# Kernel optimization log

Hardware: AMD Instinct MI355X
Metric: run time of the kernel (lower is better)

The kernel has to match this reference:

```python
import jax, jax.numpy as jnp
import numpy as np

EPS = 1e-6
INF = jnp.float32(1e12)
LAM = 1.0    # self.lam in RHD
ALPHA = 0.5  # 'alpha' is undefined in the original buggy forward; standard RHD uses 0.5


def _edt_sq_last(f):
    # Exact 1D squared distance transform along the last axis via min-plus
    # with the parabola cost (i-j)^2. f: [..., n] -> [..., n].
    n = f.shape[-1]
    idx = jnp.arange(n, dtype=f.dtype)
    d2 = (idx[:, None] - idx[None, :]) ** 2  # [n, n]
    return jnp.min(f[..., None, :] + d2, axis=-1)


def edt_sq(mask):
    # Squared Euclidean distance to nearest False pixel (scipy distance_transform_edt**2).
    # mask: bool [B, H, W]. Batched via lax.map to bound the [H, W, W] intermediate.
    f = jnp.where(mask, INF, jnp.float32(0.0))

    def one(fb):  # fb: [H, W]
        g = _edt_sq_last(fb)                 # pass along W
        d2 = _edt_sq_last(g.T).T             # pass along H
        return jnp.minimum(d2, INF)

    d2 = jax.lax.map(one, f)
    # compute_dtm leaves the map at 0 when the foreground mask is empty
    any_fg = jnp.any(mask, axis=(1, 2))
    return jnp.where(any_fg[:, None, None], d2, jnp.float32(0.0))


def setup_inputs() -> dict:
    key = jax.random.key(0)
    k1, k2 = jax.random.split(key)
    B, C, H, W = 8, 2, 512, 512
    logits = jax.random.normal(k1, (B, C, H, W), dtype=jnp.float32)
    outputs = jax.nn.softmax(logits, axis=1)  # module expects softmax results
    lab = jax.random.randint(k2, (B, H, W), 0, 2, dtype=jnp.int32)
    label_batch = jnp.stack([1 - lab, lab], axis=1)  # (B, 2, H, W) one-hot
    return {"outputs": outputs, "label_batch": label_batch}


def reference(outputs, label_batch):
    lab1_i = label_batch[:, 1]                      # (B, H, W) int
    lab1 = lab1_i.astype(outputs.dtype)

    # ---- HD loss (distance maps are constants: computed under no_grad) ----
    gt_d2 = edt_sq(lab1_i > 0)                      # (B, H, W) squared DTM of GT
    seg_d2 = edt_sq(outputs[:, 1] > 0.5)            # squared DTM of thresholded seg
    delta_s = (outputs[:, 1] - lab1) ** 2
    hd_loss = jnp.mean(delta_s * (seg_d2 + gt_d2))

    # ---- Dice loss on foreground channel ----
    score = outputs[:, 1]
    intersect = jnp.sum(score * lab1)
    denom = jnp.sum(score * score) + jnp.sum(lab1 * lab1)
    dice_loss = 1.0 - (2.0 * intersect + EPS) / (denom + EPS)

    # ---- Cross entropy: F.cross_entropy(outputs, label_batch[:,1].long()) ----
    logp = jax.nn.log_softmax(outputs, axis=1)      # (B, 2, H, W)
    picked = jnp.take_along_axis(logp, lab1_i[:, None].astype(jnp.int32), axis=1)[:, 0]
    ce_loss = -jnp.mean(picked)

    return LAM * (ce_loss + dice_loss) + (1.0 - ALPHA) * hd_loss
```

## Files before the change

### kernel.cpp

```cpp
#include <hip/hip_runtime.h>
#include <math.h>
#include <stdint.h>

#define INF_F 1.0e12f
#define NB 8
#define HW 512
#define PLANE (HW*HW)
#define NPIX (NB*PLANE)

__device__ __attribute__((noinline)) int exactRecompute(
    const float* __restrict__ outputs, const int* __restrict__ labels,
    int b, int z, int y, int x)
{
  const int base = (b*2 + 1)*PLANE;
  int m = 0x7fffffff;
  for (int ady = 0; ady < HW; ++ady) {
    if (ady*ady >= m) break;
    for (int sgn = 0; sgn < 2; ++sgn) {
      if (sgn && ady == 0) break;
      const int yy = sgn ? (y - ady) : (y + ady);
      if (yy < 0 || yy >= HW) continue;
      const int rb = base + yy*HW;
      const int a2 = ady*ady;
      for (int t = 0; t < HW; ++t) {
        const int c2 = a2 + t*t;
        if (c2 >= m) break;
        bool hit = false;
        const int xl = x - t, xr = x + t;
        if (xl >= 0)
          hit = (z == 0) ? (labels[rb + xl] <= 0) : !(outputs[rb + xl] > 0.5f);
        if (!hit && xr < HW)
          hit = (z == 0) ? (labels[rb + xr] <= 0) : !(outputs[rb + xr] > 0.5f);
        if (hit) { m = c2; break; }
      }
    }
  }
  return m;
}

__device__ __forceinline__ void visitRow(uint64_t w, int px, int a2,
                                         int pL2, int pR2, int& m, int& U)
{
  const uint64_t below = w & (~0ULL >> (63 - px));
  const uint64_t above = w >> px;
  if (below) { const int dL = px - (63 - __builtin_clzll(below)); m = min(m, a2 + dL*dL); }
  else        U = min(U, a2 + pL2);
  if (above) { const int dR = __builtin_ctzll(above); m = min(m, a2 + dR*dR); }
  else        U = min(U, a2 + pR2);
}

__device__ __forceinline__ float scanPixel(const uint64_t* __restrict__ W,
    int ry, int px, const float* __restrict__ outputs, const int* __restrict__ labels,
    int b, int z, int y, int x)
{
  const int pL2 = (px + 1)*(px + 1);
  const int pR2 = (48 - px)*(48 - px);
  int m = 0x7fffffff, U = 0x7fffffff;
  visitRow(W[ry], px, 0, pL2, pR2, m, U);
  int ady = 1;
  for (; ady <= 8; ++ady) {
    const int a2 = ady*ady;
    if (a2 >= m) break;
    visitRow(W[ry - ady], px, a2, pL2, pR2, m, U);
    visitRow(W[ry + ady], px, a2, pL2, pR2, m, U);
  }
  if (ady == 9) U = min(U, 81);
  if (m > U) {
    m = exactRecompute(outputs, labels, b, z, y, x);
    if (m == 0x7fffffff) return INF_F;
  }
  return (float)m;
}

__global__ __launch_bounds__(256) void fused_loss(
    const float* __restrict__ outputs, const int* __restrict__ labels,
    double* __restrict__ accum)
{
  __shared__ unsigned short l16[2][48][4];
  __shared__ uint64_t W[2][48];
  __shared__ double wred[4][5];
  const int tid = threadIdx.x;
  const int x0 = blockIdx.x * 32, y0 = blockIdx.y * 32, b = blockIdx.z;
  const int base1 = (b*2 + 1)*PLANE;

  for (int idx = tid; idx < 288; idx += 256) {
    const int z = idx / 144, rem = idx % 144;
    const int row = rem / 3, ch = rem % 3;
    const int yy = y0 - 8 + row;
    const int xs = x0 - 8 + ch*16;
    uint32_t bits = 0;
    if (yy >= 0 && yy < HW) {
      const int rb = base1 + yy*HW;
      if (xs >= 0 && xs + 16 <= HW) {
        if (z == 0) {
          const int4* p = (const int4*)(labels + rb + xs);
          const int4 a = p[0], c = p[1], d = p[2], e = p[3];
          const int v[16] = {a.x,a.y,a.z,a.w, c.x,c.y,c.z,c.w,
                             d.x,d.y,d.z,d.w, e.x,e.y,e.z,e.w};
#pragma unroll
          for (int t = 0; t < 16; ++t) if (v[t] <= 0) bits |= (1u << t);
        } else {
          const float4* p = (const float4*)(outputs + rb + xs);
          const float4 a = p[0], c = p[1], d = p[2], e = p[3];
          const float v[16] = {a.x,a.y,a.z,a.w, c.x,c.y,c.z,c.w,
                               d.x,d.y,d.z,d.w, e.x,e.y,e.z,e.w};
#pragma unroll
          for (int t = 0; t < 16; ++t) if (!(v[t] > 0.5f)) bits |= (1u << t);
        }
      } else {
        for (int t = 0; t < 16; ++t) {
          const int xx = xs + t;
          if (xx < 0 || xx >= HW) continue;
          const bool bg = (z == 0) ? (labels[rb + xx] <= 0)
                                   : !(outputs[rb + xx] > 0.5f);
          if (bg) bits |= (1u << t);
        }
      }
    }
    l16[z][row][ch] = (unsigned short)bits;
  }
  __syncthreads();
  if (tid < 96) {
    const int z = tid / 48, row = tid % 48;
    W[z][row] = (uint64_t)l16[z][row][0]
              | ((uint64_t)l16[z][row][1] << 16)
              | ((uint64_t)l16[z][row][2] << 32);
  }
  __syncthreads();

  const int lx = tid & 31, lyb = tid >> 5;
  const int px = 8 + lx;
  const int x = x0 + lx;
  double part = 0, dI = 0, dP2 = 0, dLs = 0, dCE = 0;
#pragma unroll
  for (int k = 0; k < 4; ++k) {
    const int ly = lyb + 8*k;
    const int y = y0 + ly;
    const int ry = 8 + ly;
    const float d2g = scanPixel(W[0], ry, px, outputs, labels, b, 0, y, x);
    const float d2s = scanPixel(W[1], ry, px, outputs, labels, b, 1, y, x);
    const int off = base1 + y*HW + x;
    const float p1  = outputs[off];
    const float p0v = outputs[off - PLANE];
    const int   lv  = labels[off];
    const float labf = (lv > 0) ? 1.0f : 0.0f;
    const float dl = p1 - labf;
    part += (double)(dl*dl*d2g) + (double)(dl*dl*d2s);
    dI  += (double)(p1 * labf);
    dP2 += (double)(p1 * p1);
    dLs += (double)labf;
    const float mm  = fmaxf(p0v, p1);
    const float lse = mm + logf(expf(p0v - mm) + expf(p1 - mm));
    dCE += (double)(((lv > 0) ? p1 : p0v) - lse);
  }

  for (int off = 32; off > 0; off >>= 1) {
    part += __shfl_down(part, off, 64);
    dI   += __shfl_down(dI,   off, 64);
    dP2  += __shfl_down(dP2,  off, 64);
    dLs  += __shfl_down(dLs,  off, 64);
    dCE  += __shfl_down(dCE,  off, 64);
  }
  const int w = tid >> 6;
  if ((tid & 63) == 0) {
    wred[w][0] = part; wred[w][1] = dI; wred[w][2] = dP2; wred[w][3] = dLs; wred[w][4] = dCE;
  }
  __syncthreads();
  if (tid < 5) {
    atomicAdd(&accum[tid], wred[0][tid] + wred[1][tid] + wred[2][tid] + wred[3][tid]);
  }
}

__global__ void finalize(const double* __restrict__ accum, float* __restrict__ out)
{
  const double N = (double)NPIX;
  const double hd   = accum[0] / N;
  const double I    = accum[1], P2 = accum[2], L = accum[3], CE = accum[4];
  const double ce   = -(CE / N);
  const double dice = 1.0 - (2.0*I + 1e-6) / (P2 + L + 1e-6);
  out[0] = (float)(ce + dice + 0.5 * hd);
}

extern "C" void kernel_launch(void* const* d_in, const int* in_sizes, int n_in,
                              void* d_out, int out_size, void* d_ws, size_t ws_size,
                              hipStream_t stream)
{
  const float* outputs = (const float*)d_in[0];
  const int*   labels  = (const int*)d_in[1];
  double* accum = (double*)d_ws;

  hipMemsetAsync(d_ws, 0, 64, stream);
  fused_loss<<<dim3(16, 16, NB), 256, 0, stream>>>(outputs, labels, accum);
  finalize<<<1, 1, 0, stream>>>(accum, (float*)d_out);
}
```

Measured before the change: 104.4 us.

## Reuse per-row horizontal distances across vertical pixel strips and drop atomics

Each thread now handles four vertically adjacent pixels and computes each row's nearest-background horizontal distance once with branchless clz/ctz, then combines rows within +/-3 to get the 2D squared distance. The exact fallback fires when the local minimum exceeds 16. The per-pixel accumulation moves from double to float with fast exp/log intrinsics. Per-block partials are written to the workspace and reduced by a 256-thread finalize kernel, which removes the memset and the atomics. The fallback window is smaller and float accumulation can cost precision.

```diff
diff --git a/kernel.cpp b/kernel.cpp
--- a/kernel.cpp
+++ b/kernel.cpp
@@ -7,6 +7,7 @@
 #define HW 512
 #define PLANE (HW*HW)
 #define NPIX (NB*PLANE)
+#define NBLK (16*16*NB)
 
 __device__ __attribute__((noinline)) int exactRecompute(
     const float* __restrict__ outputs, const int* __restrict__ labels,
@@ -38,43 +39,9 @@
   return m;
 }
 
-__device__ __forceinline__ void visitRow(uint64_t w, int px, int a2,
-                                         int pL2, int pR2, int& m, int& U)
-{
-  const uint64_t below = w & (~0ULL >> (63 - px));
-  const uint64_t above = w >> px;
-  if (below) { const int dL = px - (63 - __builtin_clzll(below)); m = min(m, a2 + dL*dL); }
-  else        U = min(U, a2 + pL2);
-  if (above) { const int dR = __builtin_ctzll(above); m = min(m, a2 + dR*dR); }
-  else        U = min(U, a2 + pR2);
-}
-
-__device__ __forceinline__ float scanPixel(const uint64_t* __restrict__ W,
-    int ry, int px, const float* __restrict__ outputs, const int* __restrict__ labels,
-    int b, int z, int y, int x)
-{
-  const int pL2 = (px + 1)*(px + 1);
-  const int pR2 = (48 - px)*(48 - px);
-  int m = 0x7fffffff, U = 0x7fffffff;
-  visitRow(W[ry], px, 0, pL2, pR2, m, U);
-  int ady = 1;
-  for (; ady <= 8; ++ady) {
-    const int a2 = ady*ady;
-    if (a2 >= m) break;
-    visitRow(W[ry - ady], px, a2, pL2, pR2, m, U);
-    visitRow(W[ry + ady], px, a2, pL2, pR2, m, U);
-  }
-  if (ady == 9) U = min(U, 81);
-  if (m > U) {
-    m = exactRecompute(outputs, labels, b, z, y, x);
-    if (m == 0x7fffffff) return INF_F;
-  }
-  return (float)m;
-}
-
 __global__ __launch_bounds__(256) void fused_loss(
     const float* __restrict__ outputs, const int* __restrict__ labels,
-    double* __restrict__ accum)
+    double* __restrict__ partials)
 {
   __shared__ unsigned short l16[2][48][4];
   __shared__ uint64_t W[2][48];
@@ -129,56 +96,108 @@
   __syncthreads();
 
   const int lx = tid & 31, lyb = tid >> 5;
-  const int px = 8 + lx;
+  const int px = 8 + lx, sh = 63 - px;
   const int x = x0 + lx;
-  double part = 0, dI = 0, dP2 = 0, dLs = 0, dCE = 0;
+  const int ry0 = 8 + lyb*4;
+
+  float d2m[2][4];
+#pragma unroll
+  for (int z = 0; z < 2; ++z) {
+    const uint64_t* __restrict__ Wz = W[z];
+    int rd2[10];
+#pragma unroll
+    for (int j = 0; j < 10; ++j) {
+      const uint64_t w = Wz[ry0 - 3 + j];
+      const int dL = __builtin_clzll((w << sh) | 1ull);
+      const int dR = __builtin_ctzll((w >> px) | (1ull << 63));
+      const int d = min(dL, dR);
+      rd2[j] = d*d;
+    }
+#pragma unroll
+    for (int k = 0; k < 4; ++k) {
+      int m = rd2[k+3];
+      m = min(m, 1 + min(rd2[k+2], rd2[k+4]));
+      m = min(m, 4 + min(rd2[k+1], rd2[k+5]));
+      m = min(m, 9 + min(rd2[k+0], rd2[k+6]));
+      float d2;
+      if (__builtin_expect(m > 16, 0)) {
+        const int mr = exactRecompute(outputs, labels, b, z, y0 + lyb*4 + k, x);
+        d2 = (mr == 0x7fffffff) ? INF_F : (float)mr;
+      } else {
+        d2 = (float)m;
+      }
+      d2m[z][k] = d2;
+    }
+  }
+
+  float part = 0, fI = 0, fP2 = 0, fL = 0, fCE = 0;
 #pragma unroll
   for (int k = 0; k < 4; ++k) {
-    const int ly = lyb + 8*k;
-    const int y = y0 + ly;
-    const int ry = 8 + ly;
-    const float d2g = scanPixel(W[0], ry, px, outputs, labels, b, 0, y, x);
-    const float d2s = scanPixel(W[1], ry, px, outputs, labels, b, 1, y, x);
+    const int y = y0 + lyb*4 + k;
     const int off = base1 + y*HW + x;
     const float p1  = outputs[off];
     const float p0v = outputs[off - PLANE];
     const int   lv  = labels[off];
     const float labf = (lv > 0) ? 1.0f : 0.0f;
     const float dl = p1 - labf;
-    part += (double)(dl*dl*d2g) + (double)(dl*dl*d2s);
-    dI  += (double)(p1 * labf);
-    dP2 += (double)(p1 * p1);
-    dLs += (double)labf;
+    part = fmaf(dl*dl, d2m[0][k] + d2m[1][k], part);
+    fI   = fmaf(p1, labf, fI);
+    fP2  = fmaf(p1, p1, fP2);
+    fL  += labf;
     const float mm  = fmaxf(p0v, p1);
-    const float lse = mm + logf(expf(p0v - mm) + expf(p1 - mm));
-    dCE += (double)(((lv > 0) ? p1 : p0v) - lse);
-  }
-
+    const float lse = mm + __logf(1.0f + __expf(fminf(p0v, p1) - mm));
+    fCE += ((lv > 0) ? p1 : p0v) - lse;
+  }
+
+  double s0 = part, s1 = fI, s2 = fP2, s3 = fL, s4 = fCE;
   for (int off = 32; off > 0; off >>= 1) {
-    part += __shfl_down(part, off, 64);
-    dI   += __shfl_down(dI,   off, 64);
-    dP2  += __shfl_down(dP2,  off, 64);
-    dLs  += __shfl_down(dLs,  off, 64);
-    dCE  += __shfl_down(dCE,  off, 64);
+    s0 += __shfl_down(s0, off, 64);
+    s1 += __shfl_down(s1, off, 64);
+    s2 += __shfl_down(s2, off, 64);
+    s3 += __shfl_down(s3, off, 64);
+    s4 += __shfl_down(s4, off, 64);
   }
   const int w = tid >> 6;
   if ((tid & 63) == 0) {
-    wred[w][0] = part; wred[w][1] = dI; wred[w][2] = dP2; wred[w][3] = dLs; wred[w][4] = dCE;
+    wred[w][0] = s0; wred[w][1] = s1; wred[w][2] = s2; wred[w][3] = s3; wred[w][4] = s4;
   }
   __syncthreads();
   if (tid < 5) {
-    atomicAdd(&accum[tid], wred[0][tid] + wred[1][tid] + wred[2][tid] + wred[3][tid]);
-  }
-}
-
-__global__ void finalize(const double* __restrict__ accum, float* __restrict__ out)
-{
-  const double N = (double)NPIX;
-  const double hd   = accum[0] / N;
-  const double I    = accum[1], P2 = accum[2], L = accum[3], CE = accum[4];
-  const double ce   = -(CE / N);
-  const double dice = 1.0 - (2.0*I + 1e-6) / (P2 + L + 1e-6);
-  out[0] = (float)(ce + dice + 0.5 * hd);
+    const int bid = (blockIdx.z*16 + blockIdx.y)*16 + blockIdx.x;
+    partials[tid*NBLK + bid] =
+        wred[0][tid] + wred[1][tid] + wred[2][tid] + wred[3][tid];
+  }
+}
+
+__global__ __launch_bounds__(256) void finalize(
+    const double* __restrict__ partials, float* __restrict__ out)
+{
+  __shared__ double wred[4][5];
+  const int tid = threadIdx.x;
+  double s[5] = {0, 0, 0, 0, 0};
+  for (int i = tid; i < NBLK; i += 256) {
+#pragma unroll
+    for (int q = 0; q < 5; ++q) s[q] += partials[q*NBLK + i];
+  }
+  for (int off = 32; off > 0; off >>= 1) {
+#pragma unroll
+    for (int q = 0; q < 5; ++q) s[q] += __shfl_down(s[q], off, 64);
+  }
+  const int w = tid >> 6;
+  if ((tid & 63) == 0) {
+#pragma unroll
+    for (int q = 0; q < 5; ++q) wred[w][q] = s[q];
+  }
+  __syncthreads();
+  if (tid == 0) {
+#pragma unroll
+    for (int q = 0; q < 5; ++q) s[q] = wred[0][q] + wred[1][q] + wred[2][q] + wred[3][q];
+    const double N = (double)NPIX;
+    const double hd   = s[0] / N;
+    const double ce   = -(s[4] / N);
+    const double dice = 1.0 - (2.0*s[1] + 1e-6) / (s[2] + s[3] + 1e-6);
+    out[0] = (float)(ce + dice + 0.5 * hd);
+  }
 }
 
 extern "C" void kernel_launch(void* const* d_in, const int* in_sizes, int n_in,
@@ -187,9 +206,8 @@
 {
   const float* outputs = (const float*)d_in[0];
   const int*   labels  = (const int*)d_in[1];
-  double* accum = (double*)d_ws;
-
-  hipMemsetAsync(d_ws, 0, 64, stream);
-  fused_loss<<<dim3(16, 16, NB), 256, 0, stream>>>(outputs, labels, accum);
-  finalize<<<1, 1, 0, stream>>>(accum, (float*)d_out);
-}
+  double* partials = (double*)d_ws;
+
+  fused_loss<<<dim3(16, 16, NB), 256, 0, stream>>>(outputs, labels, partials);
+  finalize<<<1, 256, 0, stream>>>(partials, (float*)d_out);
+}
```

New measurement: 92.79 us. 1.12x faster.
